# Kernel optimization log

Hardware: AMD Instinct MI355X
Metric: run time of the kernel (lower is better)

Reference implementation:

```python
import jax, jax.numpy as jnp
import numpy as np

D_MODEL = 1024
NUM_HEADS = 16


def setup_inputs() -> dict:
    key = jax.random.key(0)
    kx, kq, kk, kv, ko = jax.random.split(key, 5)
    B, S, D = 4, 2048, D_MODEL
    scale = 0.02
    x = jax.random.normal(kx, (B, S, D), dtype=jnp.float32)
    wq = jax.random.normal(kq, (D, D), dtype=jnp.float32) * scale
    wk = jax.random.normal(kk, (D, D), dtype=jnp.float32) * scale
    wv = jax.random.normal(kv, (D, D), dtype=jnp.float32) * scale
    wo = jax.random.normal(ko, (D, D), dtype=jnp.float32) * scale
    return {"x": x, "wq": wq, "wk": wk, "wv": wv, "wo": wo}


def reference(x, wq, wk, wv, wo):
    B, S, D = x.shape
    H = NUM_HEADS
    dk = D // H
    # projections: weight is [out, in] -> y = x @ W^T
    q = jnp.einsum('bsd,ed->bse', x, wq).reshape(B, S, H, dk).transpose(0, 2, 1, 3)
    k = jnp.einsum('bsd,ed->bse', x, wk).reshape(B, S, H, dk).transpose(0, 2, 1, 3)
    v = jnp.einsum('bsd,ed->bse', x, wv).reshape(B, S, H, dk).transpose(0, 2, 1, 3)
    # scaled dot-product attention with causal mask, [B,H,S,S]
    scores = jnp.einsum('bhqd,bhkd->bhqk', q, k) / jnp.sqrt(jnp.asarray(dk, x.dtype))
    causal = jnp.tril(jnp.ones((S, S), dtype=bool))
    scores = jnp.where(causal, scores, -jnp.inf)
    attn = jax.nn.softmax(scores, axis=-1)
    out = jnp.einsum('bhqk,bhkd->bhqd', attn, v)
    out = out.transpose(0, 2, 1, 3).reshape(B, S, D)
    return jnp.einsum('bse,de->bsd', out, wo)
```

## Files before the change

kernel.cpp:

```cpp
#include <hip/hip_runtime.h>

#define SEQ 2048
#define DM 1024
#define NH 16
#define DKH 64

typedef __attribute__((ext_vector_type(8))) short short8;
typedef __attribute__((ext_vector_type(4))) float f32x4;
typedef __attribute__((ext_vector_type(16))) float f32x16;
typedef __attribute__((ext_vector_type(2))) unsigned int u32x2;
typedef __attribute__((ext_vector_type(4))) unsigned int u32x4;

static __device__ __forceinline__ unsigned short f2b(float f) {
  unsigned int u = __float_as_uint(f);
  u += 0x7fffu + ((u >> 16) & 1u);
  return (unsigned short)(u >> 16);
}

static __device__ __forceinline__ short8 ldfrag_bf(const unsigned short* p) {
  return *reinterpret_cast<const short8*>(p);
}
static __device__ __forceinline__ short8 ldfrag_f32(const float* p) {
  const float4* q = reinterpret_cast<const float4*>(p);
  float4 a = q[0], b = q[1];
  short8 r;
  r[0] = (short)f2b(a.x); r[1] = (short)f2b(a.y);
  r[2] = (short)f2b(a.z); r[3] = (short)f2b(a.w);
  r[4] = (short)f2b(b.x); r[5] = (short)f2b(b.y);
  r[6] = (short)f2b(b.z); r[7] = (short)f2b(b.w);
  return r;
}

static __device__ __forceinline__ void gl_lds16(const void* g, void* l) {
  __builtin_amdgcn_global_load_lds(
      (const __attribute__((address_space(1))) unsigned int*)g,
      (__attribute__((address_space(3))) unsigned int*)l, 16, 0, 0);
}

__global__ __launch_bounds__(256) void zero_f32(float* __restrict__ p, int n4) {
  int i = blockIdx.x * 256 + threadIdx.x;
  if (i < n4) {
    float4 z = {0.f, 0.f, 0.f, 0.f};
    reinterpret_cast<float4*>(p)[i] = z;
  }
}

__global__ __launch_bounds__(256) void cast_f32_bf16(const float* __restrict__ src,
                                                     unsigned short* __restrict__ dst,
                                                     int n4) {
  int i = blockIdx.x * 256 + threadIdx.x;
  if (i < n4) {
    float4 v = reinterpret_cast<const float4*>(src)[i];
    ushort4 o;
    o.x = f2b(v.x); o.y = f2b(v.y); o.z = f2b(v.z); o.w = f2b(v.w);
    reinterpret_cast<ushort4*>(dst)[i] = o;
  }
}

__global__ __launch_bounds__(256) void cast4_w(const float* __restrict__ a, const float* __restrict__ b,
                                               const float* __restrict__ c, const float* __restrict__ d,
                                               unsigned short* __restrict__ oa, unsigned short* __restrict__ ob,
                                               unsigned short* __restrict__ oc, unsigned short* __restrict__ od) {
  int which = blockIdx.x >> 10;
  int i = (blockIdx.x & 1023) * 256 + threadIdx.x;
  const float* s = (which == 0) ? a : (which == 1) ? b : (which == 2) ? c : d;
  unsigned short* o = (which == 0) ? oa : (which == 1) ? ob : (which == 2) ? oc : od;
  float sc = (which == 0) ? 0.125f : 1.0f;
  float4 v = reinterpret_cast<const float4*>(s)[i];
  ushort4 u;
  u.x = f2b(v.x * sc); u.y = f2b(v.y * sc); u.z = f2b(v.z * sc); u.w = f2b(v.w * sc);
  reinterpret_cast<ushort4*>(o)[i] = u;
}

__global__ __launch_bounds__(256) void gemm_qkv(const unsigned short* __restrict__ A,
                                                const unsigned short* __restrict__ Wq,
                                                const unsigned short* __restrict__ Wk,
                                                const unsigned short* __restrict__ Wv,
                                                unsigned short* __restrict__ Qb,
                                                unsigned short* __restrict__ Kb,
                                                unsigned short* __restrict__ Vt) {
  __shared__ char smem[32768];
  unsigned short* At = (unsigned short*)smem;
  unsigned short* Wt = (unsigned short*)(smem + 16384);
  int t = threadIdx.x;
  int lane = t & 63;
  int w = t >> 6;
  int l16 = lane & 15, q4 = lane >> 4;
  int swz = (blockIdx.x & 7) * 192 + (blockIdx.x >> 3);
  int mode = swz % 3;
  int bid = swz / 3;
  int mt = bid >> 3, nt = bid & 7;
  int m0 = mt * 128, n0 = nt * 128;
  int mw = (w & 1) * 64, nw = (w >> 1) * 64;
  const unsigned short* W = (mode == 0) ? Wq : (mode == 1) ? Wk : Wv;

  const f32x4 zero4 = {0.f, 0.f, 0.f, 0.f};
  f32x4 acc[4][4];
#pragma unroll
  for (int mi = 0; mi < 4; ++mi)
#pragma unroll
    for (int nj = 0; nj < 4; ++nj) acc[mi][nj] = zero4;

  int rl0 = t >> 2, cp = t & 3;
  int rl1 = rl0 + 64;
  int sw0 = ((cp - rl0 - (rl0 >> 2)) & 3) * 8;
  int sw1 = ((cp - rl1 - (rl1 >> 2)) & 3) * 8;
  const unsigned short* ga0 = A + (long)(m0 + rl0) * DM + sw0;
  const unsigned short* ga1 = A + (long)(m0 + rl1) * DM + sw1;
  const unsigned short* gw0 = W + (long)(n0 + rl0) * DM + sw0;
  const unsigned short* gw1 = W + (long)(n0 + rl1) * DM + sw1;
  char* lA = (char*)At + t * 16;
  char* lW = (char*)Wt + t * 16;

  int aoff[4], woff[4];
#pragma unroll
  for (int mi = 0; mi < 4; ++mi) {
    int r = mw + mi * 16 + l16;
    aoff[mi] = r * 32 + ((q4 + r + (r >> 2)) & 3) * 8;
  }
#pragma unroll
  for (int nj = 0; nj < 4; ++nj) {
    int r = nw + nj * 16 + l16;
    woff[nj] = r * 32 + ((q4 + r + (r >> 2)) & 3) * 8;
  }

  gl_lds16(ga0, lA); gl_lds16(ga1, lA + 4096);
  gl_lds16(gw0, lW); gl_lds16(gw1, lW + 4096);

  for (int ks = 0; ks < 32; ++ks) {
    __syncthreads();
    if (ks + 1 < 32) {
      ga0 += 32; ga1 += 32; gw0 += 32; gw1 += 32;
      int bo = ((ks + 1) & 1) * 8192;
      gl_lds16(ga0, lA + bo); gl_lds16(ga1, lA + bo + 4096);
      gl_lds16(gw0, lW + bo); gl_lds16(gw1, lW + bo + 4096);
    }
    const unsigned short* Ab = At + (ks & 1) * 4096;
    const unsigned short* Wb = Wt + (ks & 1) * 4096;

    short8 af[4], wf[4];
#pragma unroll
    for (int mi = 0; mi < 4; ++mi) af[mi] = ldfrag_bf(Ab + aoff[mi]);
#pragma unroll
    for (int nj = 0; nj < 4; ++nj) wf[nj] = ldfrag_bf(Wb + woff[nj]);
#pragma unroll
    for (int mi = 0; mi < 4; ++mi)
#pragma unroll
      for (int nj = 0; nj < 4; ++nj)
        acc[mi][nj] = __builtin_amdgcn_mfma_f32_16x16x32_bf16(af[mi], wf[nj], acc[mi][nj], 0, 0, 0);
  }

  if (mode != 2) {
    unsigned short* o = (mode == 0) ? Qb : Kb;
#pragma unroll
    for (int mi = 0; mi < 4; ++mi)
#pragma unroll
      for (int nj = 0; nj < 4; ++nj)
#pragma unroll
        for (int r = 0; r < 4; ++r) {
          int m = m0 + mw + mi * 16 + q4 * 4 + r;
          int n = n0 + nw + nj * 16 + l16;
          int b = m >> 11, s = m & 2047;
          int h = n >> 6, d = n & 63;
          long bh = (long)(b * NH + h);
          o[(bh * SEQ + s) * DKH + d] = f2b(acc[mi][nj][r]);
        }
  } else {
    __syncthreads();
    unsigned short* vle = (unsigned short*)(smem + w * 8192);
    unsigned int* vle32 = (unsigned int*)vle;
#pragma unroll
    for (int nj = 0; nj < 4; ++nj) {
      int d = nj * 16 + l16;
      int k8 = (d & 7) * 8;
#pragma unroll
      for (int mi = 0; mi < 4; ++mi)
#pragma unroll
        for (int r = 0; r < 4; r += 2) {
          int s = mi * 16 + q4 * 4 + r;
          unsigned int pk = (unsigned int)f2b(acc[mi][nj][r]) |
                            ((unsigned int)f2b(acc[mi][nj][r + 1]) << 16);
          vle32[d * 32 + ((s ^ k8) >> 1)] = pk;
        }
    }
    __asm__ volatile("s_waitcnt lgkmcnt(0)" ::: "memory");
    int b = m0 >> 11;
    int h = (n0 + nw) >> 6;
    long bh = (long)(b * NH + h);
    int sbase = (m0 + mw) & 2047;
    int dr_lo = lane >> 3, c = lane & 7;
#pragma unroll
    for (int pass = 0; pass < 8; ++pass) {
      int dr = pass * 8 + dr_lo;
      int cc = c ^ (dr & 7);
      short8 vv = ldfrag_bf(vle + dr * 64 + cc * 8);
      *reinterpret_cast<short8*>(Vt + (bh * DKH + dr) * SEQ + sbase + c * 8) = vv;
    }
  }
}

__global__ __launch_bounds__(256) void gemm_o(const unsigned short* __restrict__ A,
                                              const unsigned short* __restrict__ W,
                                              float* __restrict__ outp) {
  __shared__ char smem[32768];
  unsigned short* At = (unsigned short*)smem;
  unsigned short* Wt = (unsigned short*)(smem + 16384);
  int t = threadIdx.x;
  int lane = t & 63;
  int w = t >> 6;
  int l16 = lane & 15, q4 = lane >> 4;
  int swz = (blockIdx.x & 7) * 64 + (blockIdx.x >> 3);
  int mt = swz >> 3, nt = swz & 7;
  int m0 = mt * 128, n0 = nt * 128;
  int mw = (w & 1) * 64, nw = (w >> 1) * 64;

  const f32x4 zero4 = {0.f, 0.f, 0.f, 0.f};
  f32x4 acc[4][4];
#pragma unroll
  for (int mi = 0; mi < 4; ++mi)
#pragma unroll
    for (int nj = 0; nj < 4; ++nj) acc[mi][nj] = zero4;

  int rl0 = t >> 2, cp = t & 3;
  int rl1 = rl0 + 64;
  int sw0 = ((cp - rl0 - (rl0 >> 2)) & 3) * 8;
  int sw1 = ((cp - rl1 - (rl1 >> 2)) & 3) * 8;
  int b0 = m0 >> 11;
  const unsigned short* ga0;
  const unsigned short* ga1;
  {
    int s0 = (m0 & 2047) + rl0;
    ga0 = A + (long)b0 * (NH * SEQ * DKH) + (long)s0 * DKH + sw0;
    int s1 = (m0 & 2047) + rl1;
    ga1 = A + (long)b0 * (NH * SEQ * DKH) + (long)s1 * DKH + sw1;
  }
  const unsigned short* gw0 = W + (long)(n0 + rl0) * DM + sw0;
  const unsigned short* gw1 = W + (long)(n0 + rl1) * DM + sw1;
  char* lA = (char*)At + t * 16;
  char* lW = (char*)Wt + t * 16;

  int aoff[4], woff[4];
#pragma unroll
  for (int mi = 0; mi < 4; ++mi) {
    int r = mw + mi * 16 + l16;
    aoff[mi] = r * 32 + ((q4 + r + (r >> 2)) & 3) * 8;
  }
#pragma unroll
  for (int nj = 0; nj < 4; ++nj) {
    int r = nw + nj * 16 + l16;
    woff[nj] = r * 32 + ((q4 + r + (r >> 2)) & 3) * 8;
  }

  gl_lds16(ga0, lA); gl_lds16(ga1, lA + 4096);
  gl_lds16(gw0, lW); gl_lds16(gw1, lW + 4096);

  for (int ks = 0; ks < 32; ++ks) {
    __syncthreads();
    if (ks + 1 < 32) {
      int adv = ((ks & 1) == 0) ? 32 : (SEQ * DKH - 32);
      ga0 += adv; ga1 += adv; gw0 += 32; gw1 += 32;
      int bo = ((ks + 1) & 1) * 8192;
      gl_lds16(ga0, lA + bo); gl_lds16(ga1, lA + bo + 4096);
      gl_lds16(gw0, lW + bo); gl_lds16(gw1, lW + bo + 4096);
    }
    const unsigned short* Ab = At + (ks & 1) * 4096;
    const unsigned short* Wb = Wt + (ks & 1) * 4096;

    short8 af[4], wf[4];
#pragma unroll
    for (int mi = 0; mi < 4; ++mi) af[mi] = ldfrag_bf(Ab + aoff[mi]);
#pragma unroll
    for (int nj = 0; nj < 4; ++nj) wf[nj] = ldfrag_bf(Wb + woff[nj]);
#pragma unroll
    for (int mi = 0; mi < 4; ++mi)
#pragma unroll
      for (int nj = 0; nj < 4; ++nj)
        acc[mi][nj] = __builtin_amdgcn_mfma_f32_16x16x32_bf16(af[mi], wf[nj], acc[mi][nj], 0, 0, 0);
  }

#pragma unroll
  for (int mi = 0; mi < 4; ++mi)
#pragma unroll
    for (int nj = 0; nj < 4; ++nj)
#pragma unroll
      for (int r = 0; r < 4; ++r) {
        int m = m0 + mw + mi * 16 + q4 * 4 + r;
        int n = n0 + nw + nj * 16 + l16;
        outp[(long)m * DM + n] = acc[mi][nj][r];
      }
}

template<int MODE, bool AF32, bool WF32>
__global__ __launch_bounds__(256) void gemm_s(const void* __restrict__ Ap,
                                              const void* __restrict__ Wp,
                                              void* __restrict__ outp) {
  int wid  = (blockIdx.x * 256 + threadIdx.x) >> 6;
  int lane = threadIdx.x & 63;
  int l16  = lane & 15, q4 = lane >> 4;
  int tn = wid & 15, tm = wid >> 4;
  int m0 = tm * 32, n0 = tn * 64;

  const float*          Af = (const float*)Ap;
  const unsigned short* Ab = (const unsigned short*)Ap;
  const float*          Wf = (const float*)Wp;
  const unsigned short* Wb = (const unsigned short*)Wp;

  const f32x4 zero4 = {0.f, 0.f, 0.f, 0.f};
  f32x4 acc[2][4];
#pragma unroll
  for (int mi = 0; mi < 2; ++mi)
#pragma unroll
    for (int j = 0; j < 4; ++j) acc[mi][j] = zero4;

  int wrow[4];
#pragma unroll
  for (int j = 0; j < 4; ++j) wrow[j] = (n0 + j * 16 + l16) * DM;
  int arow[2] = {0, 0};
  long abase[2] = {0, 0};
  if (MODE != 3) {
#pragma unroll
    for (int mi = 0; mi < 2; ++mi) arow[mi] = (m0 + mi * 16 + l16) * DM;
  } else {
    int b = m0 >> 11;
#pragma unroll
    for (int mi = 0; mi < 2; ++mi) {
      int srow = (m0 & 2047) + mi * 16 + l16;
      abase[mi] = (long)b * (NH * SEQ * DKH) + (long)srow * DKH;
    }
  }

#pragma unroll 2
  for (int ks = 0; ks < 32; ++ks) {
    int ko = ks * 32 + q4 * 8;
    short8 bfrag[4];
#pragma unroll
    for (int j = 0; j < 4; ++j) {
      if constexpr (WF32) bfrag[j] = ldfrag_f32(Wf + wrow[j] + ko);
      else                bfrag[j] = ldfrag_bf(Wb + wrow[j] + ko);
    }
    short8 afrag[2];
    if constexpr (MODE != 3) {
#pragma unroll
      for (int mi = 0; mi < 2; ++mi) {
        if constexpr (AF32) afrag[mi] = ldfrag_f32(Af + arow[mi] + ko);
        else                afrag[mi] = ldfrag_bf(Ab + arow[mi] + ko);
      }
    } else {
      int h = ko >> 6, e63 = ko & 63;
#pragma unroll
      for (int mi = 0; mi < 2; ++mi)
        afrag[mi] = ldfrag_bf(Ab + abase[mi] + (long)h * (SEQ * DKH) + e63);
    }
#pragma unroll
    for (int mi = 0; mi < 2; ++mi)
#pragma unroll
      for (int j = 0; j < 4; ++j)
        acc[mi][j] = __builtin_amdgcn_mfma_f32_16x16x32_bf16(afrag[mi], bfrag[j], acc[mi][j], 0, 0, 0);
  }

#pragma unroll
  for (int mi = 0; mi < 2; ++mi) {
#pragma unroll
    for (int j = 0; j < 4; ++j) {
#pragma unroll
      for (int r = 0; r < 4; ++r) {
        float v = acc[mi][j][r];
        int m = m0 + mi * 16 + q4 * 4 + r;
        int n = n0 + j * 16 + l16;
        if constexpr (MODE == 3) {
          reinterpret_cast<float*>(outp)[(long)m * DM + n] = v;
        } else {
          int b = m >> 11, s = m & 2047;
          int h = n >> 6, d = n & 63;
          long bh = (long)(b * NH + h);
          unsigned short* o = reinterpret_cast<unsigned short*>(outp);
          if constexpr (MODE == 0)      o[(bh * SEQ + s) * DKH + d] = f2b(v * 0.125f);
          else if constexpr (MODE == 1) o[(bh * SEQ + s) * DKH + d] = f2b(v);
          else                          o[(bh * DKH + d) * SEQ + s] = f2b(v);
        }
      }
    }
  }
}

__global__ __launch_bounds__(256, 4) void attn_k(const unsigned short* __restrict__ Kbuf,
                                                 const unsigned short* __restrict__ Vt,
                                                 const unsigned short* __restrict__ Qbuf,
                                                 unsigned short* __restrict__ Obuf) {
  __shared__ unsigned short Kt[2][64 * 64];
  __shared__ unsigned short Vts[2][64 * 64];

  int t = threadIdx.x;
  int lane = t & 63;
  int w = t >> 6;
  int l31 = lane & 31, hi = lane >> 5;
  int qb = 15 - (blockIdx.x >> 6);
  int bh = blockIdx.x & 63;
  int q0 = qb * 128;
  int qw0 = q0 + w * 32;

  const unsigned short* Qh = Qbuf + (long)bh * (SEQ * DKH);
  const unsigned short* Kh = Kbuf + (long)bh * (SEQ * DKH);
  const unsigned short* Vh = Vt   + (long)bh * (DKH * SEQ);

  short8 qf[4];
#pragma unroll
  for (int dt = 0; dt < 4; ++dt)
    qf[dt] = ldfrag_bf(Qh + (long)(qw0 + l31) * DKH + dt * 16 + hi * 8);

  f32x16 om[2];
#pragma unroll
  for (int dv = 0; dv < 2; ++dv)
#pragma unroll
    for (int r = 0; r < 16; ++r) om[dv][r] = 0.f;
  float lsum = 0.f;

  int koff[2][4];
#pragma unroll
  for (int sub = 0; sub < 2; ++sub) {
    int kr = sub * 32 + l31;
#pragma unroll
    for (int dt = 0; dt < 4; ++dt)
      koff[sub][dt] = kr * 64 + ((dt * 2 + hi + kr + (kr >> 3)) & 7) * 8;
  }
  int voff[2][4];
#pragma unroll
  for (int dv = 0; dv < 2; ++dv) {
    int dr = dv * 32 + l31;
#pragma unroll
    for (int kc = 0; kc < 4; ++kc)
      voff[dv][kc] = dr * 64 + ((kc * 2 + hi + dr + (dr >> 3)) & 7) * 8;
  }

  int rl0 = t >> 3, cp = t & 7;
  int rl1 = rl0 + 32;
  int sw0 = ((cp - rl0 - (rl0 >> 3)) & 7) * 8;
  int sw1 = ((cp - rl1 - (rl1 >> 3)) & 7) * 8;
  const unsigned short* kp0 = Kh + (long)rl0 * DKH + sw0;
  const unsigned short* kp1 = Kh + (long)rl1 * DKH + sw1;
  const unsigned short* vp0 = Vh + (long)rl0 * SEQ + sw0;
  const unsigned short* vp1 = Vh + (long)rl1 * SEQ + sw1;
  char* lK = (char*)Kt + t * 16;
  char* lV = (char*)Vts + t * 16;

  int nk = 2 * qb + 2;
  gl_lds16(kp0, lK); gl_lds16(kp1, lK + 4096);
  gl_lds16(vp0, lV); gl_lds16(vp1, lV + 4096);

  for (int it = 0; it < nk; ++it) {
    __syncthreads();
    if (it + 1 < nk) {
      kp0 += 64 * DKH; kp1 += 64 * DKH; vp0 += 64; vp1 += 64;
      int bo = ((it + 1) & 1) * 8192;
      gl_lds16(kp0, lK + bo); gl_lds16(kp1, lK + bo + 4096);
      gl_lds16(vp0, lV + bo); gl_lds16(vp1, lV + bo + 4096);
    }

    int k0 = it * 64;
    if (k0 <= qw0 + 31) {
      const unsigned short* KT = Kt[0] + (it & 1) * 4096;
      const unsigned short* VT = Vts[0] + (it & 1) * 4096;

#pragma unroll
      for (int sub = 0; sub < 2; ++sub) {
        int ksb = k0 + sub * 32;
        if (ksb <= qw0 + 31) {
          f32x16 s;
#pragma unroll
          for (int r = 0; r < 16; ++r) s[r] = 0.f;
#pragma unroll
          for (int dt = 0; dt < 4; ++dt) {
            short8 kf = ldfrag_bf(KT + koff[sub][dt]);
            s = __builtin_amdgcn_mfma_f32_32x32x16_bf16(kf, qf[dt], s, 0, 0, 0);
          }

          bool needmask = (ksb + 31 > qw0);
          int qr = qw0 + l31;
          unsigned int pk[4][2];
#pragma unroll
          for (int r = 0; r < 16; r += 2) {
            float p0 = __expf(s[r]);
            float p1 = __expf(s[r + 1]);
            if (needmask) {
              int key = ksb + (r & 3) + 8 * (r >> 2) + 4 * hi;
              p0 = (key <= qr) ? p0 : 0.f;
              p1 = (key + 1 <= qr) ? p1 : 0.f;
            }
            unsigned int u0 = __float_as_uint(p0) & 0xffff0000u;
            unsigned int u1 = __float_as_uint(p1) & 0xffff0000u;
            lsum += __uint_as_float(u0) + __uint_as_float(u1);
            pk[r >> 2][(r >> 1) & 1] = (u0 >> 16) | u1;
          }

#pragma unroll
          for (int c = 0; c < 2; ++c) {
            u32x2 r0 = __builtin_amdgcn_permlane32_swap(pk[2 * c][0], pk[2 * c + 1][0], false, false);
            u32x2 r1 = __builtin_amdgcn_permlane32_swap(pk[2 * c][1], pk[2 * c + 1][1], false, false);
            u32x4 pw;
            pw.x = r0.x; pw.y = r1.x; pw.z = r0.y; pw.w = r1.y;
            short8 pa = __builtin_bit_cast(short8, pw);
            int kc = sub * 2 + c;
#pragma unroll
            for (int dv = 0; dv < 2; ++dv) {
              short8 vf = ldfrag_bf(VT + voff[dv][kc]);
              om[dv] = __builtin_amdgcn_mfma_f32_32x32x16_bf16(pa, vf, om[dv], 0, 0, 0);
            }
          }
        }
      }
    }
  }

  u32x2 lz = __builtin_amdgcn_permlane32_swap(__float_as_uint(lsum), __float_as_uint(lsum),
                                              false, false);
  float inv = 1.f / (__uint_as_float(lz.x) + __uint_as_float(lz.y));

  long obase = (long)bh * (SEQ * DKH);
#pragma unroll
  for (int r = 0; r < 16; ++r) {
    int qrow = (r & 3) + 8 * (r >> 2) + 4 * hi;
    float invq = __shfl(inv, qrow);
    long rowb = obase + (long)(qw0 + qrow) * DKH + l31;
    Obuf[rowb]      = f2b(om[0][r] * invq);
    Obuf[rowb + 32] = f2b(om[1][r] * invq);
  }
}

extern "C" void kernel_launch(void* const* d_in, const int* in_sizes, int n_in,
                              void* d_out, int out_size, void* d_ws, size_t ws_size,
                              hipStream_t stream) {
  const float* x  = (const float*)d_in[0];
  const float* wq = (const float*)d_in[1];
  const float* wk = (const float*)d_in[2];
  const float* wv = (const float*)d_in[3];
  const float* wo = (const float*)d_in[4];

  unsigned short* Qb = (unsigned short*)d_out;
  unsigned short* Kb = Qb + 8388608;

  if (ws_size >= 41943040ull) {
    unsigned short* xb  = (unsigned short*)d_ws;
    unsigned short* wqb = xb + 8388608;
    unsigned short* wkb = wqb + 1048576;
    unsigned short* wvb = wkb + 1048576;
    unsigned short* wob = wvb + 1048576;
    unsigned short* Vt  = wob + 1048576;
    unsigned short* Ob  = xb;

    cast_f32_bf16<<<8192, 256, 0, stream>>>(x, xb, 2097152);
    cast4_w<<<4096, 256, 0, stream>>>(wq, wk, wv, wo, wqb, wkb, wvb, wob);

    gemm_qkv<<<1536, 256, 0, stream>>>(xb, wqb, wkb, wvb, Qb, Kb, Vt);
    attn_k<<<1024, 256, 0, stream>>>(Kb, Vt, Qb, Ob);
    gemm_o<<<512, 256, 0, stream>>>(Ob, wob, (float*)d_out);
  } else if (ws_size >= 33554432ull) {
    unsigned short* Vt = (unsigned short*)d_ws;
    unsigned short* Ob = Vt + 8388608;

    gemm_s<0, true, true><<<1024, 256, 0, stream>>>(x, wq, Qb);
    gemm_s<1, true, true><<<1024, 256, 0, stream>>>(x, wk, Kb);
    gemm_s<2, true, true><<<1024, 256, 0, stream>>>(x, wv, Vt);
    attn_k<<<1024, 256, 0, stream>>>(Kb, Vt, Qb, Ob);
    gemm_s<3, false, true><<<1024, 256, 0, stream>>>(Ob, wo, d_out);
  } else {
    zero_f32<<<8192, 256, 0, stream>>>((float*)d_out, 2097152);
  }
}
```

Measured before the change: 248.2 us.

## Merge cast kernels, drop QKV block swizzle, precompute epilogue store addresses

Combines the activation cast and the four weight casts into a single launch, saving one kernel launch and the gap between them. Removes the XCD-aware block swizzle in the QKV GEMM and uses a plain modulo-3 block mapping instead. Replaces per-element index arithmetic in the Q/K, V-transpose and output-projection epilogues with precomputed base pointers and constant offsets. Dropping the swizzle may reduce L2 locality across chiplets.

Measured after the change: 252.0 us. Within noise of the previous version (+1.5%).

```diff
diff --git a/kernel.cpp b/kernel.cpp
--- a/kernel.cpp
+++ b/kernel.cpp
@@ -45,31 +45,31 @@
   }
 }
 
-__global__ __launch_bounds__(256) void cast_f32_bf16(const float* __restrict__ src,
-                                                     unsigned short* __restrict__ dst,
-                                                     int n4) {
-  int i = blockIdx.x * 256 + threadIdx.x;
-  if (i < n4) {
-    float4 v = reinterpret_cast<const float4*>(src)[i];
+__global__ __launch_bounds__(256) void cast_all(const float* __restrict__ x,
+                                                const float* __restrict__ a, const float* __restrict__ b,
+                                                const float* __restrict__ c, const float* __restrict__ d,
+                                                unsigned short* __restrict__ xo,
+                                                unsigned short* __restrict__ oa, unsigned short* __restrict__ ob,
+                                                unsigned short* __restrict__ oc, unsigned short* __restrict__ od) {
+  int blk = blockIdx.x;
+  if (blk < 8192) {
+    int i = blk * 256 + threadIdx.x;
+    float4 v = reinterpret_cast<const float4*>(x)[i];
     ushort4 o;
     o.x = f2b(v.x); o.y = f2b(v.y); o.z = f2b(v.z); o.w = f2b(v.w);
-    reinterpret_cast<ushort4*>(dst)[i] = o;
-  }
-}
-
-__global__ __launch_bounds__(256) void cast4_w(const float* __restrict__ a, const float* __restrict__ b,
-                                               const float* __restrict__ c, const float* __restrict__ d,
-                                               unsigned short* __restrict__ oa, unsigned short* __restrict__ ob,
-                                               unsigned short* __restrict__ oc, unsigned short* __restrict__ od) {
-  int which = blockIdx.x >> 10;
-  int i = (blockIdx.x & 1023) * 256 + threadIdx.x;
-  const float* s = (which == 0) ? a : (which == 1) ? b : (which == 2) ? c : d;
-  unsigned short* o = (which == 0) ? oa : (which == 1) ? ob : (which == 2) ? oc : od;
-  float sc = (which == 0) ? 0.125f : 1.0f;
-  float4 v = reinterpret_cast<const float4*>(s)[i];
-  ushort4 u;
-  u.x = f2b(v.x * sc); u.y = f2b(v.y * sc); u.z = f2b(v.z * sc); u.w = f2b(v.w * sc);
-  reinterpret_cast<ushort4*>(o)[i] = u;
+    reinterpret_cast<ushort4*>(xo)[i] = o;
+  } else {
+    blk -= 8192;
+    int which = blk >> 10;
+    int i = (blk & 1023) * 256 + threadIdx.x;
+    const float* s = (which == 0) ? a : (which == 1) ? b : (which == 2) ? c : d;
+    unsigned short* o = (which == 0) ? oa : (which == 1) ? ob : (which == 2) ? oc : od;
+    float sc = (which == 0) ? 0.125f : 1.0f;
+    float4 v = reinterpret_cast<const float4*>(s)[i];
+    ushort4 u;
+    u.x = f2b(v.x * sc); u.y = f2b(v.y * sc); u.z = f2b(v.z * sc); u.w = f2b(v.w * sc);
+    reinterpret_cast<ushort4*>(o)[i] = u;
+  }
 }
 
 __global__ __launch_bounds__(256) void gemm_qkv(const unsigned short* __restrict__ A,
@@ -86,9 +86,8 @@
   int lane = t & 63;
   int w = t >> 6;
   int l16 = lane & 15, q4 = lane >> 4;
-  int swz = (blockIdx.x & 7) * 192 + (blockIdx.x >> 3);
-  int mode = swz % 3;
-  int bid = swz / 3;
+  int mode = blockIdx.x % 3;
+  int bid = blockIdx.x / 3;
   int mt = bid >> 3, nt = bid & 7;
   int m0 = mt * 128, n0 = nt * 128;
   int mw = (w & 1) * 64, nw = (w >> 1) * 64;
@@ -152,19 +151,17 @@
 
   if (mode != 2) {
     unsigned short* o = (mode == 0) ? Qb : Kb;
+    int b = m0 >> 11;
+    int h = (n0 + nw) >> 6;
+    long bh0 = (long)(b * NH + h);
+    unsigned short* op = o + (bh0 * SEQ + (m0 & 2047) + mw + q4 * 4) * DKH + l16;
 #pragma unroll
     for (int mi = 0; mi < 4; ++mi)
 #pragma unroll
       for (int nj = 0; nj < 4; ++nj)
 #pragma unroll
-        for (int r = 0; r < 4; ++r) {
-          int m = m0 + mw + mi * 16 + q4 * 4 + r;
-          int n = n0 + nw + nj * 16 + l16;
-          int b = m >> 11, s = m & 2047;
-          int h = n >> 6, d = n & 63;
-          long bh = (long)(b * NH + h);
-          o[(bh * SEQ + s) * DKH + d] = f2b(acc[mi][nj][r]);
-        }
+        for (int r = 0; r < 4; ++r)
+          op[mi * 1024 + r * 64 + nj * 16] = f2b(acc[mi][nj][r]);
   } else {
     __syncthreads();
     unsigned short* vle = (unsigned short*)(smem + w * 8192);
@@ -189,12 +186,12 @@
     long bh = (long)(b * NH + h);
     int sbase = (m0 + mw) & 2047;
     int dr_lo = lane >> 3, c = lane & 7;
+    const unsigned short* vr = vle + dr_lo * 64 + (c ^ dr_lo) * 8;
+    unsigned short* vtp = Vt + (bh * DKH + dr_lo) * SEQ + sbase + c * 8;
 #pragma unroll
     for (int pass = 0; pass < 8; ++pass) {
-      int dr = pass * 8 + dr_lo;
-      int cc = c ^ (dr & 7);
-      short8 vv = ldfrag_bf(vle + dr * 64 + cc * 8);
-      *reinterpret_cast<short8*>(Vt + (bh * DKH + dr) * SEQ + sbase + c * 8) = vv;
+      short8 vv = ldfrag_bf(vr + pass * 512);
+      *reinterpret_cast<short8*>(vtp + (long)pass * 8 * SEQ) = vv;
     }
   }
 }
@@ -278,16 +275,16 @@
         acc[mi][nj] = __builtin_amdgcn_mfma_f32_16x16x32_bf16(af[mi], wf[nj], acc[mi][nj], 0, 0, 0);
   }
 
-#pragma unroll
-  for (int mi = 0; mi < 4; ++mi)
-#pragma unroll
-    for (int nj = 0; nj < 4; ++nj)
-#pragma unroll
-      for (int r = 0; r < 4; ++r) {
-        int m = m0 + mw + mi * 16 + q4 * 4 + r;
-        int n = n0 + nw + nj * 16 + l16;
-        outp[(long)m * DM + n] = acc[mi][nj][r];
-      }
+  {
+    float* op = outp + (long)(m0 + mw + q4 * 4) * DM + n0 + nw + l16;
+#pragma unroll
+    for (int mi = 0; mi < 4; ++mi)
+#pragma unroll
+      for (int nj = 0; nj < 4; ++nj)
+#pragma unroll
+        for (int r = 0; r < 4; ++r)
+          op[(mi * 16 + r) * DM + nj * 16] = acc[mi][nj][r];
+  }
 }
 
 template<int MODE, bool AF32, bool WF32>
@@ -547,8 +544,7 @@
     unsigned short* Vt  = wob + 1048576;
     unsigned short* Ob  = xb;
 
-    cast_f32_bf16<<<8192, 256, 0, stream>>>(x, xb, 2097152);
-    cast4_w<<<4096, 256, 0, stream>>>(wq, wk, wv, wo, wqb, wkb, wvb, wob);
+    cast_all<<<12288, 256, 0, stream>>>(x, wq, wk, wv, wo, xb, wqb, wkb, wvb, wob);
 
     gemm_qkv<<<1536, 256, 0, stream>>>(xb, wqb, wkb, wvb, Qb, Kb, Vt);
     attn_k<<<1024, 256, 0, stream>>>(Kb, Vt, Qb, Ob);
```
